# Performance work log

Hardware: AMD Instinct MI355X
Metric: run time of the kernel (lower is better)

Reference implementation:

```python
import jax, jax.numpy as jnp
import numpy as np
from jax import lax


def setup_inputs() -> dict:
    key = jax.random.key(0)
    ks = jax.random.split(key, 3)
    T, B, IC, HC, L = 512, 64, 1024, 1024, 2
    # xavier_normal-ish scale for square layers
    scale = (2.0 / (IC + HC)) ** 0.5
    x = jax.random.normal(ks[0], (T, B, IC), dtype=jnp.float32)
    Wi = jax.random.normal(ks[1], (L, HC, IC), dtype=jnp.float32) * scale
    Wh = jax.random.normal(ks[2], (L, HC, HC), dtype=jnp.float32) * scale
    bi = jnp.zeros((L, HC), dtype=jnp.float32)
    bh = jnp.zeros((L, HC), dtype=jnp.float32)
    return {"x": x, "Wi": Wi, "bi": bi, "Wh": Wh, "bh": bh}


def _run_rnn(x, Wi, bi, Wh, bh):
    # x: [T, B, ic]; Wi: [L, hc, ic]; Wh: [L, hc, hc]
    L = Wi.shape[0]
    B = x.shape[1]
    HC = Wh.shape[-1]
    seq = x
    finals = []
    for i in range(L):  # small fixed layer count
        # precompute input projection for all timesteps (one big GEMM)
        pre = jnp.einsum('tbi,hi->tbh', seq, Wi[i]) + bi[i]
        Wh_i, bh_i = Wh[i], bh[i]

        def step(h, p):
            h_new = jnp.tanh(p + h @ Wh_i.T + bh_i)
            return h_new, h_new

        h0 = jnp.zeros((B, HC), dtype=x.dtype)  # hiddens=None, learn_init=False
        h_last, seq = lax.scan(step, h0, pre)
        finals.append(h_last)
    hs = jnp.stack(finals, axis=0)  # [L, B, hc]
    return seq, hs


def reference(x, Wi, bi, Wh, bh):
    out, hs = _run_rnn(x, Wi, bi, Wh, bh)
    return out, hs
```

## Files before the change

kernel.cpp:

```cpp
#include <hip/hip_runtime.h>


#define T_STEPS 512
#define HCC     1024
#define BH      65536
#define NWG     192

typedef __attribute__((ext_vector_type(8))) short  bf16x8;
typedef __attribute__((ext_vector_type(4))) float  f32x4;

#define WF_SHORTS   8388608u
#define SLAB_SHORTS 131072u
#define OFF_H1F     WF_SHORTS
#define OFF_H2F     (OFF_H1F + 4u*SLAB_SHORTS)
#define OFF_PRE2_BYTES ((size_t)(OFF_H2F + 4u*SLAB_SHORTS) * 2u)
#define PRE2_FLOATS 65536u
#define FLG_BYTE_OFF (OFF_PRE2_BYTES + 4u*(size_t)PRE2_FLOATS*4u)
#define FLG_UINTS   (3u*64u*4u*4u)

__device__ __forceinline__ unsigned fidx(unsigned g, unsigned i, unsigned wp) {
    return ((g * 64u + i) * 4u + wp) * 4u;
}

__device__ __forceinline__ void gload_b128_cc(bf16x8& d, const unsigned short* p) {
    asm volatile("global_load_dwordx4 %0, %1, off sc0 sc1" : "=v"(d) : "v"(p));
}
__device__ __forceinline__ void gload_f128_cc(f32x4& d, const float* p) {
    asm volatile("global_load_dwordx4 %0, %1, off sc0 sc1" : "=v"(d) : "v"(p));
}
__device__ __forceinline__ void gload_f128_nc(f32x4& d, const float* p) {
    asm volatile("global_load_dwordx4 %0, %1, off" : "=v"(d) : "v"(p));
}
__device__ __forceinline__ void gstore_b128_cc(bf16x8 v, unsigned short* p) {
    asm volatile("global_store_dwordx4 %0, %1, off sc0 sc1" :: "v"(p), "v"(v) : "memory");
}
__device__ __forceinline__ void gstore_f128_cc(f32x4 v, float* p) {
    asm volatile("global_store_dwordx4 %0, %1, off sc0 sc1" :: "v"(p), "v"(v) : "memory");
}
__device__ __forceinline__ void vm_drain()  { asm volatile("s_waitcnt vmcnt(0)"  ::: "memory"); }
__device__ __forceinline__ void vm_wait2()  { asm volatile("s_waitcnt vmcnt(2)"  ::: "memory"); }
__device__ __forceinline__ void vm_wait4()  { asm volatile("s_waitcnt vmcnt(4)"  ::: "memory"); }
__device__ __forceinline__ void vm_wait8()  { asm volatile("s_waitcnt vmcnt(8)"  ::: "memory"); }
__device__ __forceinline__ void vm_wait12() { asm volatile("s_waitcnt vmcnt(12)" ::: "memory"); }
#define SBAR() __builtin_amdgcn_sched_barrier(0)

__device__ __forceinline__ unsigned short bf16_rne_bits(float f) {
    unsigned u = __builtin_bit_cast(unsigned, f);
    unsigned r = u + 0x7fffu + ((u >> 16) & 1u);
    return (unsigned short)(r >> 16);
}
__device__ __forceinline__ void split1(float f, unsigned short& hi, unsigned short& lo) {
    unsigned u = __builtin_bit_cast(unsigned, f);
    unsigned r = (u + 0x7fffu + ((u >> 16) & 1u)) & 0xffff0000u;
    hi = (unsigned short)(r >> 16);
    float res = f - __builtin_bit_cast(float, r);
    lo = bf16_rne_bits(res);
}
__device__ __forceinline__ void split8(const float* f, bf16x8& H, bf16x8& L) {
#pragma unroll
    for (int e = 0; e < 8; ++e) {
        unsigned short hi, lo; split1(f[e], hi, lo);
        H[e] = (short)hi; L[e] = (short)lo;
    }
}
__device__ __forceinline__ float tanh_fast(float v) {
    float e = __expf(2.0f * v);
    return 1.0f - 2.0f * __builtin_amdgcn_rcpf(e + 1.0f);
}

__global__ __launch_bounds__(256) void zero_cnt_kernel(unsigned* cnt, unsigned n) {
    unsigned i = blockIdx.x * 256u + threadIdx.x;
    if (i < n) cnt[i] = 0u;
}

__global__ __launch_bounds__(256) void wsplit_kernel(
    const float* __restrict__ Wi, const float* __restrict__ Wh,
    unsigned short* __restrict__ WF)
{
    unsigned id  = blockIdx.x * 256u + threadIdx.x;
    unsigned kc  = id & 127u;
    unsigned row = (id >> 7) & 1023u;
    unsigned m   = id >> 17;

    const float* src = ((m & 1u) ? Wh : Wi) + (size_t)(m >> 1) * HCC * HCC
                     + (size_t)row * HCC + kc * 8u;
    float f[8];
    *(f32x4*)&f[0] = *(const f32x4*)&src[0];
    *(f32x4*)&f[4] = *(const f32x4*)&src[4];
    bf16x8 H, L; split8(f, H, L);

    unsigned c16 = row >> 4, ks = kc >> 2;
    unsigned lane = (row & 15u) + 16u * (kc & 3u);
    size_t bh_ = (((size_t)(m * 2u + 0u) * 64u + c16) * 32u + ks) * 512u + lane * 8u;
    size_t bl_ = (((size_t)(m * 2u + 1u) * 64u + c16) * 32u + ks) * 512u + lane * 8u;
    *(bf16x8*)&WF[bh_] = H;
    *(bf16x8*)&WF[bl_] = L;
}

__global__ __launch_bounds__(256) void pre1_gemm(
    const float* __restrict__ x, const float* __restrict__ bi, const float* __restrict__ bh,
    const unsigned short* __restrict__ WF, float* __restrict__ preO)
{
    __shared__ float xs[64 * 36];
    const unsigned t = blockIdx.x >> 3, cg = blockIdx.x & 7u;
    const unsigned tid = threadIdx.x, w = tid >> 6, lane = tid & 63u;
    const unsigned ct32 = cg * 4u + w;

    float b0 = bi[ct32 * 32u + (lane & 15u)]        + bh[ct32 * 32u + (lane & 15u)];
    float b1 = bi[ct32 * 32u + 16u + (lane & 15u)]  + bh[ct32 * 32u + 16u + (lane & 15u)];
    f32x4 acc[4][2];
#pragma unroll
    for (unsigned rt = 0; rt < 4; ++rt) {
        acc[rt][0] = (f32x4){b0, b0, b0, b0};
        acc[rt][1] = (f32x4){b1, b1, b1, b1};
    }
    const float* xt = x + (size_t)t * BH;

    for (unsigned ks = 0; ks < 32; ++ks) {
        {
            unsigned row = tid >> 2, c8 = (tid & 3u) * 8u;
            const float* sp = xt + (size_t)row * HCC + ks * 32u + c8;
            *(f32x4*)&xs[row * 36u + c8]      = *(const f32x4*)&sp[0];
            *(f32x4*)&xs[row * 36u + c8 + 4u] = *(const f32x4*)&sp[4];
        }
        __syncthreads();
        bf16x8 bhv[2], blv[2];
#pragma unroll
        for (unsigned c16 = 0; c16 < 2; ++c16) {
            size_t base = (((size_t)(0u) * 64u + (ct32 * 2u + c16)) * 32u + ks) * 512u + lane * 8u;
            bhv[c16] = *(const bf16x8*)&WF[base];
            blv[c16] = *(const bf16x8*)&WF[base + (size_t)64u * 32u * 512u];
        }
#pragma unroll
        for (unsigned rt = 0; rt < 4; ++rt) {
            unsigned row = rt * 16u + (lane & 15u);
            unsigned k0 = (lane >> 4) * 8u;
            float f[8];
            *(f32x4*)&f[0] = *(const f32x4*)&xs[row * 36u + k0];
            *(f32x4*)&f[4] = *(const f32x4*)&xs[row * 36u + k0 + 4u];
            bf16x8 ah, al; split8(f, ah, al);
#pragma unroll
            for (unsigned c16 = 0; c16 < 2; ++c16) {
                acc[rt][c16] = __builtin_amdgcn_mfma_f32_16x16x32_bf16(ah, bhv[c16], acc[rt][c16], 0, 0, 0);
                acc[rt][c16] = __builtin_amdgcn_mfma_f32_16x16x32_bf16(al, bhv[c16], acc[rt][c16], 0, 0, 0);
                acc[rt][c16] = __builtin_amdgcn_mfma_f32_16x16x32_bf16(ah, blv[c16], acc[rt][c16], 0, 0, 0);
            }
        }
        __syncthreads();
    }
#pragma unroll
    for (unsigned rt = 0; rt < 4; ++rt)
#pragma unroll
        for (unsigned c16 = 0; c16 < 2; ++c16) {
            unsigned rh = rt >> 1, fi = (rt & 1u) * 2u + c16;
            size_t off = ((((size_t)t * 2u + rh) * 32u + ct32) * 4u + fi) * 256u + lane * 4u;
            *(f32x4*)&preO[off] = acc[rt][c16];
        }
}

__global__ __launch_bounds__(512, 1) void rnn_persist(
    const float* __restrict__ bi, const float* __restrict__ bh,
    const unsigned short* __restrict__ WF,
    unsigned short* __restrict__ h1F, unsigned short* __restrict__ h2F,
    float* __restrict__ pre2F, unsigned* __restrict__ flg,
    float* __restrict__ seqO, float* __restrict__ hsO)
{
    __shared__ short WlS[65536];
    __shared__ float redS[7168];
    float* const epS = &redS[4096];

    const unsigned wg  = blockIdx.x;
    const unsigned grp = wg >> 6;
    const unsigned sub = wg & 63u;
    const unsigned rh  = sub >> 5, ct = sub & 31u;
    const unsigned tid = threadIdx.x;
    const unsigned w   = tid >> 6, lane = tid & 63u;

    const unsigned mat = grp + 1u;
#pragma unroll
    for (unsigned prec = 0; prec < 2; ++prec)
#pragma unroll
        for (unsigned c16l = 0; c16l < 2; ++c16l) {
            const unsigned short* sp = WF + (((size_t)(mat * 2u + prec) * 64u + (ct * 2u + c16l)) * 32u) * 512u;
            short* dp = &WlS[(prec * 2u + c16l) * 16384u];
            for (unsigned o = tid * 8u; o < 16384u; o += 4096u)
                *(bf16x8*)&dp[o] = *(const bf16x8*)&sp[o];
        }
    __syncthreads();

    float binit0 = 0.f, binit1 = 0.f;
    if (grp == 1u) {
        unsigned c = HCC + ct * 32u + (lane & 15u);
        binit0 = bi[c] + bh[c];
        binit1 = bi[c + 16u] + bh[c + 16u];
    }

    const int s0_ = (grp == 0u) ? 0 : (grp == 1u) ? 1 : 2;
    const int s1_ = s0_ + 511;

#define POLL16(G, TGT) do {                                                           \
        const unsigned* fp_ = flg + fidx((G), rh * 32u + w * 4u + ((lane >> 2) & 3u), \
                                         lane & 3u);                                  \
        while (!__all((int)(__hip_atomic_load(fp_, __ATOMIC_RELAXED,                  \
                                              __HIP_MEMORY_SCOPE_AGENT) >= (unsigned)(TGT)))) \
            __builtin_amdgcn_s_sleep(1);                                              \
    } while (0)
#define POLLW0(G, TGT) do {                                                           \
        const unsigned* fp_ = flg + fidx((G), lane, 0u);                              \
        while (!__all((int)(__hip_atomic_load(fp_, __ATOMIC_RELAXED,                  \
                                              __HIP_MEMORY_SCOPE_AGENT) >= (unsigned)(TGT)))) \
            __builtin_amdgcn_s_sleep(1);                                              \
    } while (0)
#define POLL1(G, IDX, TGT) do {                                                       \
        const unsigned* fp_ = flg + fidx((G), (IDX), 0u);                             \
        while (__hip_atomic_load(fp_, __ATOMIC_RELAXED,                               \
                                 __HIP_MEMORY_SCOPE_AGENT) < (unsigned)(TGT))         \
            __builtin_amdgcn_s_sleep(1);                                              \
    } while (0)

    for (int s = s0_; s <= s1_; ++s) {
        if (grp == 0u)      { if (s >= 1) POLL16(0u, s); }
        else if (grp == 1u) { POLL16(0u, s); }
        else {
            if (s >= 3) POLL16(2u, s);
            if (w == 0u) POLL1(1u, sub, s);
        }
        if (w == 1u) {
            if (grp == 0u && s >= 4) POLLW0(1u, s - 2);
            if (grp == 1u && s >= 5) POLLW0(2u, s - 2);
        }
        if (w == 2u) {
            if (grp == 0u && s >= 4) POLLW0(0u, s - 2);
            if (grp == 2u && s >= 6) POLLW0(2u, s - 2);
        }

        const bool do_h   = (grp == 0u) ? (s > 0) : (grp == 1u) ? true : (s > 2);
        const bool has_ld = (w == 0u && grp != 1u);

        bf16x8 Ah0[4], Ah1[4], Al0[4], Al1[4];
        if (do_h) {
            const unsigned aslot = (grp == 2u) ? ((unsigned)(s - 3) & 3u)
                                               : ((unsigned)(s - 1) & 3u);
            const unsigned short* Aslab = (grp <= 1u ? h1F : h2F)
                                        + (size_t)aslot * SLAB_SHORTS;
            const unsigned b00 = ((rh * 2u + 0u) * 2u + 0u) * 16384u;
            const unsigned b01 = ((rh * 2u + 0u) * 2u + 1u) * 16384u;
            const unsigned b10 = ((rh * 2u + 1u) * 2u + 0u) * 16384u;
            const unsigned b11 = ((rh * 2u + 1u) * 2u + 1u) * 16384u;
#pragma unroll
            for (unsigned i = 0; i < 4; ++i) {
                const unsigned ao = (w * 4u + i) * 512u + lane * 8u;
                gload_b128_cc(Ah0[i], Aslab + b00 + ao);
                gload_b128_cc(Ah1[i], Aslab + b01 + ao);
            }
#pragma unroll
            for (unsigned i = 0; i < 4; ++i) {
                const unsigned ao = (w * 4u + i) * 512u + lane * 8u;
                gload_b128_cc(Al0[i], Aslab + b10 + ao);
                gload_b128_cc(Al1[i], Aslab + b11 + ao);
            }
        }
        f32x4 ld0 = {0,0,0,0}, ld1 = {0,0,0,0}, ld2 = {0,0,0,0}, ld3 = {0,0,0,0};
        if (has_ld) {
            if (grp == 0u) {
                const float* pp = seqO + (((size_t)s * 2u + rh) * 32u + ct) * 1024u;
                gload_f128_nc(ld0, pp + 0u * 256u + lane * 4u);
                gload_f128_nc(ld1, pp + 1u * 256u + lane * 4u);
                gload_f128_nc(ld2, pp + 2u * 256u + lane * 4u);
                gload_f128_nc(ld3, pp + 3u * 256u + lane * 4u);
            } else {
                const float* pp = pre2F + (size_t)((s - 2) & 3) * PRE2_FLOATS
                                + ((size_t)rh * 32u + ct) * 1024u;
                gload_f128_cc(ld0, pp + 0u * 256u + lane * 4u);
                gload_f128_cc(ld1, pp + 1u * 256u + lane * 4u);
                gload_f128_cc(ld2, pp + 2u * 256u + lane * 4u);
                gload_f128_cc(ld3, pp + 3u * 256u + lane * 4u);
            }
        }

        f32x4 a00 = {0,0,0,0}, a01 = {0,0,0,0}, a10 = {0,0,0,0}, a11 = {0,0,0,0};
        if (do_h) {
            if (has_ld) vm_wait12(); else vm_wait8();
            SBAR();
#pragma unroll
            for (unsigned i = 0; i < 4; ++i) {
                const unsigned ao = (w * 4u + i) * 512u + lane * 8u;
                bf16x8 bh0 = *(const bf16x8*)&WlS[ao];
                bf16x8 bh1 = *(const bf16x8*)&WlS[16384u + ao];
                bf16x8 bl0 = *(const bf16x8*)&WlS[32768u + ao];
                bf16x8 bl1 = *(const bf16x8*)&WlS[49152u + ao];
                a00 = __builtin_amdgcn_mfma_f32_16x16x32_bf16(Ah0[i], bh0, a00, 0, 0, 0);
                a01 = __builtin_amdgcn_mfma_f32_16x16x32_bf16(Ah0[i], bh1, a01, 0, 0, 0);
                a10 = __builtin_amdgcn_mfma_f32_16x16x32_bf16(Ah1[i], bh0, a10, 0, 0, 0);
                a11 = __builtin_amdgcn_mfma_f32_16x16x32_bf16(Ah1[i], bh1, a11, 0, 0, 0);
                a00 = __builtin_amdgcn_mfma_f32_16x16x32_bf16(Ah0[i], bl0, a00, 0, 0, 0);
                a01 = __builtin_amdgcn_mfma_f32_16x16x32_bf16(Ah0[i], bl1, a01, 0, 0, 0);
                a10 = __builtin_amdgcn_mfma_f32_16x16x32_bf16(Ah1[i], bl0, a10, 0, 0, 0);
                a11 = __builtin_amdgcn_mfma_f32_16x16x32_bf16(Ah1[i], bl1, a11, 0, 0, 0);
            }
            if (has_ld) vm_wait4(); else vm_drain();
            SBAR();
#pragma unroll
            for (unsigned i = 0; i < 4; ++i) {
                const unsigned ao = (w * 4u + i) * 512u + lane * 8u;
                bf16x8 bh0 = *(const bf16x8*)&WlS[ao];
                bf16x8 bh1 = *(const bf16x8*)&WlS[16384u + ao];
                a00 = __builtin_amdgcn_mfma_f32_16x16x32_bf16(Al0[i], bh0, a00, 0, 0, 0);
                a01 = __builtin_amdgcn_mfma_f32_16x16x32_bf16(Al0[i], bh1, a01, 0, 0, 0);
                a10 = __builtin_amdgcn_mfma_f32_16x16x32_bf16(Al1[i], bh0, a10, 0, 0, 0);
                a11 = __builtin_amdgcn_mfma_f32_16x16x32_bf16(Al1[i], bh1, a11, 0, 0, 0);
            }
        } else {
            vm_drain(); SBAR();
        }

        if (w) {
            *(f32x4*)&redS[((w - 1u) * 4u + 0u) * 256u + lane * 4u] = a00;
            *(f32x4*)&redS[((w - 1u) * 4u + 1u) * 256u + lane * 4u] = a01;
            *(f32x4*)&redS[((w - 1u) * 4u + 2u) * 256u + lane * 4u] = a10;
            *(f32x4*)&redS[((w - 1u) * 4u + 3u) * 256u + lane * 4u] = a11;
        }
        __syncthreads();
        if (w == 0u) {
#pragma unroll
            for (unsigned b = 0; b < 7; ++b) {
                a00 += *(const f32x4*)&redS[(b * 4u + 0u) * 256u + lane * 4u];
                a01 += *(const f32x4*)&redS[(b * 4u + 1u) * 256u + lane * 4u];
                a10 += *(const f32x4*)&redS[(b * 4u + 2u) * 256u + lane * 4u];
                a11 += *(const f32x4*)&redS[(b * 4u + 3u) * 256u + lane * 4u];
            }
            vm_drain(); SBAR();
            if (grp == 1u) {
                a00 += (f32x4){binit0, binit0, binit0, binit0};
                a01 += (f32x4){binit1, binit1, binit1, binit1};
                a10 += (f32x4){binit0, binit0, binit0, binit0};
                a11 += (f32x4){binit1, binit1, binit1, binit1};
                float* pp = pre2F + (size_t)((s - 1) & 3) * PRE2_FLOATS
                          + ((size_t)rh * 32u + ct) * 1024u;
                gstore_f128_cc(a00, pp + 0u * 256u + lane * 4u);
                gstore_f128_cc(a01, pp + 1u * 256u + lane * 4u);
                gstore_f128_cc(a10, pp + 2u * 256u + lane * 4u);
                gstore_f128_cc(a11, pp + 3u * 256u + lane * 4u);
                vm_drain();
                if (lane == 0u)
                    __hip_atomic_store(flg + fidx(1u, sub, 0u), (unsigned)s + 1u,
                                       __ATOMIC_RELAXED, __HIP_MEMORY_SCOPE_AGENT);
            } else {
                a00 += ld0; a01 += ld1; a10 += ld2; a11 += ld3;
#pragma unroll
                for (unsigned rr = 0; rr < 4; ++rr) {
                    unsigned rbase = ((lane >> 4) * 4u + rr) * 36u;
                    epS[rbase + (lane & 15u)]                 = tanh_fast(a00[rr]);
                    epS[rbase + 16u + (lane & 15u)]           = tanh_fast(a01[rr]);
                    epS[576u + rbase + (lane & 15u)]          = tanh_fast(a10[rr]);
                    epS[576u + rbase + 16u + (lane & 15u)]    = tanh_fast(a11[rr]);
                }
            }
        }
        if (grp != 1u) {
            __syncthreads();
            if (w < 4u) {
                const unsigned r16l = w >> 1, prec = w & 1u;
                const unsigned row = r16l * 16u + (lane & 15u);
                const unsigned c0 = (lane >> 4) * 8u;
                float f[8];
                *(f32x4*)&f[0] = *(const f32x4*)&epS[row * 36u + c0];
                *(f32x4*)&f[4] = *(const f32x4*)&epS[row * 36u + c0 + 4u];
                bf16x8 H, L; split8(f, H, L);
                unsigned short* hdst = (grp == 0u ? h1F : h2F)
                    + (size_t)((unsigned)(grp == 0u ? s : s - 2) & 3u) * SLAB_SHORTS;
                gstore_b128_cc(prec ? L : H,
                    hdst + ((rh * 2u + prec) * 2u + r16l) * 16384u + ct * 512u + lane * 8u);
            }
            if (grp == 2u) {
                const int t2 = s - 2;
#pragma unroll
                for (unsigned pass = 0; pass < 2; ++pass) {
                    const unsigned r = w * 4u + pass * 2u + (lane >> 5);
                    const unsigned c = lane & 31u;
                    const float v = epS[r * 36u + c];
                    seqO[((size_t)t2 * 64u + rh * 32u + r) * 1024u + ct * 32u + c] = v;
                    if (s == 513) hsO[BH + (size_t)(rh * 32u + r) * 1024u + ct * 32u + c] = v;
                }
            }
            if (grp == 0u && s == 511) {
#pragma unroll
                for (unsigned pass = 0; pass < 2; ++pass) {
                    const unsigned r = w * 4u + pass * 2u + (lane >> 5);
                    const unsigned c = lane & 31u;
                    hsO[(size_t)(rh * 32u + r) * 1024u + ct * 32u + c] = epS[r * 36u + c];
                }
            }
            if (w < 4u) {
                if (grp == 2u && s < 513) vm_wait2(); else vm_drain();
                if (lane == 0u)
                    __hip_atomic_store(flg + fidx(grp, sub, w), (unsigned)s + 1u,
                                       __ATOMIC_RELAXED, __HIP_MEMORY_SCOPE_AGENT);
            }
        }
        __syncthreads();
    }
    vm_drain();
#undef POLL16
#undef POLLW0
#undef POLL1
}

extern "C" void kernel_launch(void* const* d_in, const int* in_sizes, int n_in,
                              void* d_out, int out_size, void* d_ws, size_t ws_size,
                              hipStream_t stream) {
    const float* x  = (const float*)d_in[0];
    const float* Wi = (const float*)d_in[1];
    const float* bi = (const float*)d_in[2];
    const float* Wh = (const float*)d_in[3];
    const float* bh = (const float*)d_in[4];

    float* seqO = (float*)d_out;
    float* hsO  = seqO + (size_t)T_STEPS * BH;

    unsigned short* wsS = (unsigned short*)d_ws;
    unsigned short* WF  = wsS;
    unsigned short* h1F = wsS + OFF_H1F;
    unsigned short* h2F = wsS + OFF_H2F;
    float* pre2F = (float*)((char*)d_ws + OFF_PRE2_BYTES);
    unsigned* flg = (unsigned*)((char*)d_ws + FLG_BYTE_OFF);

    zero_cnt_kernel<<<(FLG_UINTS + 255u) / 256u, 256, 0, stream>>>(flg, FLG_UINTS);
    wsplit_kernel<<<2048, 256, 0, stream>>>(Wi, Wh, WF);
    pre1_gemm<<<4096, 256, 0, stream>>>(x, bi, bh, WF, seqO);
    rnn_persist<<<NWG, 512, 0, stream>>>(bi, bh, WF, h1F, h2F, pre2F, flg, seqO, hsO);
}
```

Before: 2.788 ms.

## Split cross-wave reduction and epilogue across four waves, per-wave flags

The final reduction of the eight waves' MFMA partial sums is now spread across four waves, each owning one 16x16 fragment, instead of all being done by wave 0. The pre-activation loads are likewise split one per wave, and grp1 publishes per-wave flags that grp2 polls with a wave-wide check. The WAR polls (POLLW0) move from before the GEMM to after it, so they overlap compute, and the flag stores now follow the h stores immediately. The aim is to shorten the serial critical path of each recurrent step, at the cost of more flag traffic and a reshuffled shared-memory layout.

```diff
diff --git a/kernel.cpp b/kernel.cpp
--- a/kernel.cpp
+++ b/kernel.cpp
@@ -38,10 +38,7 @@
     asm volatile("global_store_dwordx4 %0, %1, off sc0 sc1" :: "v"(p), "v"(v) : "memory");
 }
 __device__ __forceinline__ void vm_drain()  { asm volatile("s_waitcnt vmcnt(0)"  ::: "memory"); }
-__device__ __forceinline__ void vm_wait2()  { asm volatile("s_waitcnt vmcnt(2)"  ::: "memory"); }
-__device__ __forceinline__ void vm_wait4()  { asm volatile("s_waitcnt vmcnt(4)"  ::: "memory"); }
 __device__ __forceinline__ void vm_wait8()  { asm volatile("s_waitcnt vmcnt(8)"  ::: "memory"); }
-__device__ __forceinline__ void vm_wait12() { asm volatile("s_waitcnt vmcnt(12)" ::: "memory"); }
 #define SBAR() __builtin_amdgcn_sched_barrier(0)
 
 __device__ __forceinline__ unsigned short bf16_rne_bits(float f) {
@@ -167,7 +164,6 @@
 {
     __shared__ short WlS[65536];
     __shared__ float redS[7168];
-    float* const epS = &redS[4096];
 
     const unsigned wg  = blockIdx.x;
     const unsigned grp = wg >> 6;
@@ -188,11 +184,10 @@
         }
     __syncthreads();
 
-    float binit0 = 0.f, binit1 = 0.f;
-    if (grp == 1u) {
-        unsigned c = HCC + ct * 32u + (lane & 15u);
-        binit0 = bi[c] + bh[c];
-        binit1 = bi[c + 16u] + bh[c + 16u];
+    float bsel = 0.f;
+    if (grp == 1u && w < 4u) {
+        unsigned c = HCC + ct * 32u + (w & 1u) * 16u + (lane & 15u);
+        bsel = bi[c] + bh[c];
     }
 
     const int s0_ = (grp == 0u) ? 0 : (grp == 1u) ? 1 : 2;
@@ -211,31 +206,34 @@
                                               __HIP_MEMORY_SCOPE_AGENT) >= (unsigned)(TGT)))) \
             __builtin_amdgcn_s_sleep(1);                                              \
     } while (0)
-#define POLL1(G, IDX, TGT) do {                                                       \
-        const unsigned* fp_ = flg + fidx((G), (IDX), 0u);                             \
-        while (__hip_atomic_load(fp_, __ATOMIC_RELAXED,                               \
-                                 __HIP_MEMORY_SCOPE_AGENT) < (unsigned)(TGT))         \
+#define POLLG1(TGT) do {                                                              \
+        const unsigned* fp_ = flg + fidx(1u, sub, lane & 3u);                         \
+        while (!__all((int)(__hip_atomic_load(fp_, __ATOMIC_RELAXED,                  \
+                                              __HIP_MEMORY_SCOPE_AGENT) >= (unsigned)(TGT)))) \
             __builtin_amdgcn_s_sleep(1);                                              \
     } while (0)
 
     for (int s = s0_; s <= s1_; ++s) {
-        if (grp == 0u)      { if (s >= 1) POLL16(0u, s); }
-        else if (grp == 1u) { POLL16(0u, s); }
-        else {
+        const bool do_h   = (grp == 0u) ? (s > 0) : (grp == 1u) ? true : (s > 2);
+
+        f32x4 ldq = {0, 0, 0, 0};
+        if (grp == 0u) {
+            if (w < 4u) {
+                const float* pp = seqO + (((size_t)s * 2u + rh) * 32u + ct) * 1024u;
+                gload_f128_nc(ldq, pp + w * 256u + lane * 4u);
+            }
+            if (s >= 1) POLL16(0u, s);
+        } else if (grp == 1u) {
+            POLL16(0u, s);
+        } else {
+            if (w < 4u) {
+                POLLG1(s);
+                const float* pp = pre2F + (size_t)((s - 2) & 3) * PRE2_FLOATS
+                                + ((size_t)rh * 32u + ct) * 1024u;
+                gload_f128_cc(ldq, pp + w * 256u + lane * 4u);
+            }
             if (s >= 3) POLL16(2u, s);
-            if (w == 0u) POLL1(1u, sub, s);
-        }
-        if (w == 1u) {
-            if (grp == 0u && s >= 4) POLLW0(1u, s - 2);
-            if (grp == 1u && s >= 5) POLLW0(2u, s - 2);
-        }
-        if (w == 2u) {
-            if (grp == 0u && s >= 4) POLLW0(0u, s - 2);
-            if (grp == 2u && s >= 6) POLLW0(2u, s - 2);
-        }
-
-        const bool do_h   = (grp == 0u) ? (s > 0) : (grp == 1u) ? true : (s > 2);
-        const bool has_ld = (w == 0u && grp != 1u);
+        }
 
         bf16x8 Ah0[4], Ah1[4], Al0[4], Al1[4];
         if (do_h) {
@@ -260,28 +258,10 @@
                 gload_b128_cc(Al1[i], Aslab + b11 + ao);
             }
         }
-        f32x4 ld0 = {0,0,0,0}, ld1 = {0,0,0,0}, ld2 = {0,0,0,0}, ld3 = {0,0,0,0};
-        if (has_ld) {
-            if (grp == 0u) {
-                const float* pp = seqO + (((size_t)s * 2u + rh) * 32u + ct) * 1024u;
-                gload_f128_nc(ld0, pp + 0u * 256u + lane * 4u);
-                gload_f128_nc(ld1, pp + 1u * 256u + lane * 4u);
-                gload_f128_nc(ld2, pp + 2u * 256u + lane * 4u);
-                gload_f128_nc(ld3, pp + 3u * 256u + lane * 4u);
-            } else {
-                const float* pp = pre2F + (size_t)((s - 2) & 3) * PRE2_FLOATS
-                                + ((size_t)rh * 32u + ct) * 1024u;
-                gload_f128_cc(ld0, pp + 0u * 256u + lane * 4u);
-                gload_f128_cc(ld1, pp + 1u * 256u + lane * 4u);
-                gload_f128_cc(ld2, pp + 2u * 256u + lane * 4u);
-                gload_f128_cc(ld3, pp + 3u * 256u + lane * 4u);
-            }
-        }
 
         f32x4 a00 = {0,0,0,0}, a01 = {0,0,0,0}, a10 = {0,0,0,0}, a11 = {0,0,0,0};
         if (do_h) {
-            if (has_ld) vm_wait12(); else vm_wait8();
-            SBAR();
+            vm_wait8(); SBAR();
 #pragma unroll
             for (unsigned i = 0; i < 4; ++i) {
                 const unsigned ao = (w * 4u + i) * 512u + lane * 8u;
@@ -298,8 +278,7 @@
                 a10 = __builtin_amdgcn_mfma_f32_16x16x32_bf16(Ah1[i], bl0, a10, 0, 0, 0);
                 a11 = __builtin_amdgcn_mfma_f32_16x16x32_bf16(Ah1[i], bl1, a11, 0, 0, 0);
             }
-            if (has_ld) vm_wait4(); else vm_drain();
-            SBAR();
+            vm_drain(); SBAR();
 #pragma unroll
             for (unsigned i = 0; i < 4; ++i) {
                 const unsigned ao = (w * 4u + i) * 512u + lane * 8u;
@@ -314,63 +293,69 @@
             vm_drain(); SBAR();
         }
 
-        if (w) {
-            *(f32x4*)&redS[((w - 1u) * 4u + 0u) * 256u + lane * 4u] = a00;
-            *(f32x4*)&redS[((w - 1u) * 4u + 1u) * 256u + lane * 4u] = a01;
-            *(f32x4*)&redS[((w - 1u) * 4u + 2u) * 256u + lane * 4u] = a10;
-            *(f32x4*)&redS[((w - 1u) * 4u + 3u) * 256u + lane * 4u] = a11;
+        if (w == 1u) {
+            if (grp == 0u && s >= 4) POLLW0(1u, s - 2);
+            if (grp == 1u && s >= 5) POLLW0(2u, s - 2);
+        }
+        if (w == 2u) {
+            if (grp == 0u && s >= 4) POLLW0(0u, s - 2);
+            if (grp == 2u && s >= 6) POLLW0(2u, s - 2);
+        }
+
+        {
+            f32x4 av[4] = {a00, a01, a10, a11};
+#pragma unroll
+            for (unsigned f = 0; f < 4; ++f) {
+                const bool skip = (w < 4u) && (f == w);
+                const unsigned wi = w - ((w > f) ? 1u : 0u);
+                if (!skip)
+                    *(f32x4*)&redS[(f * 7u + wi) * 256u + lane * 4u] = av[f];
+            }
         }
         __syncthreads();
-        if (w == 0u) {
-#pragma unroll
-            for (unsigned b = 0; b < 7; ++b) {
-                a00 += *(const f32x4*)&redS[(b * 4u + 0u) * 256u + lane * 4u];
-                a01 += *(const f32x4*)&redS[(b * 4u + 1u) * 256u + lane * 4u];
-                a10 += *(const f32x4*)&redS[(b * 4u + 2u) * 256u + lane * 4u];
-                a11 += *(const f32x4*)&redS[(b * 4u + 3u) * 256u + lane * 4u];
-            }
-            vm_drain(); SBAR();
+
+        if (w < 4u) {
+            f32x4 acc = (w == 0u) ? a00 : (w == 1u) ? a01 : (w == 2u) ? a10 : a11;
+#pragma unroll
+            for (unsigned b = 0; b < 7; ++b)
+                acc += *(const f32x4*)&redS[(w * 7u + b) * 256u + lane * 4u];
             if (grp == 1u) {
-                a00 += (f32x4){binit0, binit0, binit0, binit0};
-                a01 += (f32x4){binit1, binit1, binit1, binit1};
-                a10 += (f32x4){binit0, binit0, binit0, binit0};
-                a11 += (f32x4){binit1, binit1, binit1, binit1};
+                acc += (f32x4){bsel, bsel, bsel, bsel};
                 float* pp = pre2F + (size_t)((s - 1) & 3) * PRE2_FLOATS
                           + ((size_t)rh * 32u + ct) * 1024u;
-                gstore_f128_cc(a00, pp + 0u * 256u + lane * 4u);
-                gstore_f128_cc(a01, pp + 1u * 256u + lane * 4u);
-                gstore_f128_cc(a10, pp + 2u * 256u + lane * 4u);
-                gstore_f128_cc(a11, pp + 3u * 256u + lane * 4u);
+                gstore_f128_cc(acc, pp + w * 256u + lane * 4u);
                 vm_drain();
                 if (lane == 0u)
-                    __hip_atomic_store(flg + fidx(1u, sub, 0u), (unsigned)s + 1u,
+                    __hip_atomic_store(flg + fidx(1u, sub, w), (unsigned)s + 1u,
                                        __ATOMIC_RELAXED, __HIP_MEMORY_SCOPE_AGENT);
             } else {
-                a00 += ld0; a01 += ld1; a10 += ld2; a11 += ld3;
-#pragma unroll
-                for (unsigned rr = 0; rr < 4; ++rr) {
-                    unsigned rbase = ((lane >> 4) * 4u + rr) * 36u;
-                    epS[rbase + (lane & 15u)]                 = tanh_fast(a00[rr]);
-                    epS[rbase + 16u + (lane & 15u)]           = tanh_fast(a01[rr]);
-                    epS[576u + rbase + (lane & 15u)]          = tanh_fast(a10[rr]);
-                    epS[576u + rbase + 16u + (lane & 15u)]    = tanh_fast(a11[rr]);
-                }
+                acc += ldq;
+                const unsigned qb = w * 1792u;
+                const unsigned rb = (lane >> 4) * 4u;
+#pragma unroll
+                for (unsigned rr = 0; rr < 4; ++rr)
+                    redS[qb + (rb + rr) * 16u + (lane & 15u)] = tanh_fast(acc[rr]);
             }
         }
         if (grp != 1u) {
             __syncthreads();
             if (w < 4u) {
                 const unsigned r16l = w >> 1, prec = w & 1u;
-                const unsigned row = r16l * 16u + (lane & 15u);
                 const unsigned c0 = (lane >> 4) * 8u;
+                const unsigned q  = r16l * 2u + (c0 >> 4);
+                const unsigned qa = q * 1792u + (lane & 15u) * 16u + (c0 & 15u);
                 float f[8];
-                *(f32x4*)&f[0] = *(const f32x4*)&epS[row * 36u + c0];
-                *(f32x4*)&f[4] = *(const f32x4*)&epS[row * 36u + c0 + 4u];
+                *(f32x4*)&f[0] = *(const f32x4*)&redS[qa];
+                *(f32x4*)&f[4] = *(const f32x4*)&redS[qa + 4u];
                 bf16x8 H, L; split8(f, H, L);
                 unsigned short* hdst = (grp == 0u ? h1F : h2F)
                     + (size_t)((unsigned)(grp == 0u ? s : s - 2) & 3u) * SLAB_SHORTS;
                 gstore_b128_cc(prec ? L : H,
                     hdst + ((rh * 2u + prec) * 2u + r16l) * 16384u + ct * 512u + lane * 8u);
+                vm_drain();
+                if (lane == 0u)
+                    __hip_atomic_store(flg + fidx(grp, sub, w), (unsigned)s + 1u,
+                                       __ATOMIC_RELAXED, __HIP_MEMORY_SCOPE_AGENT);
             }
             if (grp == 2u) {
                 const int t2 = s - 2;
@@ -378,7 +363,8 @@
                 for (unsigned pass = 0; pass < 2; ++pass) {
                     const unsigned r = w * 4u + pass * 2u + (lane >> 5);
                     const unsigned c = lane & 31u;
-                    const float v = epS[r * 36u + c];
+                    const float v = redS[((r >> 4) * 2u + (c >> 4)) * 1792u
+                                         + (r & 15u) * 16u + (c & 15u)];
                     seqO[((size_t)t2 * 64u + rh * 32u + r) * 1024u + ct * 32u + c] = v;
                     if (s == 513) hsO[BH + (size_t)(rh * 32u + r) * 1024u + ct * 32u + c] = v;
                 }
@@ -388,14 +374,10 @@
                 for (unsigned pass = 0; pass < 2; ++pass) {
                     const unsigned r = w * 4u + pass * 2u + (lane >> 5);
                     const unsigned c = lane & 31u;
-                    hsO[(size_t)(rh * 32u + r) * 1024u + ct * 32u + c] = epS[r * 36u + c];
+                    hsO[(size_t)(rh * 32u + r) * 1024u + ct * 32u + c]
+                        = redS[((r >> 4) * 2u + (c >> 4)) * 1792u
+                               + (r & 15u) * 16u + (c & 15u)];
                 }
-            }
-            if (w < 4u) {
-                if (grp == 2u && s < 513) vm_wait2(); else vm_drain();
-                if (lane == 0u)
-                    __hip_atomic_store(flg + fidx(grp, sub, w), (unsigned)s + 1u,
-                                       __ATOMIC_RELAXED, __HIP_MEMORY_SCOPE_AGENT);
             }
         }
         __syncthreads();
@@ -403,7 +385,7 @@
     vm_drain();
 #undef POLL16
 #undef POLLW0
-#undef POLL1
+#undef POLLG1
 }
 
 extern "C" void kernel_launch(void* const* d_in, const int* in_sizes, int n_in,
```

Measured after the change: 2.510 ms. -10.0%, faster.
